# Performance work log

Hardware: AMD Instinct MI355X
Metric: run time of the kernel (lower is better)

## Reference

```python
import jax, jax.numpy as jnp
import numpy as np
import math

B, N, F = 16, 1024, 1024
OUT = 1024

def setup_inputs() -> dict:
    key = jax.random.key(0)
    k1, k2, k3, k4 = jax.random.split(key, 4)
    prott5_emd = jax.random.normal(k1, (B, N, F), dtype=jnp.float32)
    # shared (dense) normalized adjacency, as the original applies one adj to every sample
    adj = jax.random.uniform(k2, (N, N), dtype=jnp.float32)
    adj = adj / jnp.sum(adj, axis=1, keepdims=True)  # row-normalize like a GCN propagation matrix
    h0 = jax.random.normal(k3, (B, N, F), dtype=jnp.float32)
    stdv = 1.0 / math.sqrt(OUT)
    weight = jax.random.uniform(k4, (F, OUT), minval=-stdv, maxval=stdv, dtype=jnp.float32)
    return {"prott5_emd": prott5_emd, "adj": adj, "h0": h0, "weight": weight,
            "lamda": 0.5, "alpha": 0.1, "l": 1}

def reference(prott5_emd, adj, h0, weight, lamda, alpha, l):
    # GraphConvolution (GCNII-style), variant=False, residual=False
    theta = min(1.0, math.log(lamda / l + 1.0))  # static python scalar
    # batched aggregation: adj @ x_i for every sample i  ->  [B, N, F]
    hi = jnp.einsum('nm,bmf->bnf', adj, prott5_emd)
    support = (1.0 - alpha) * hi + alpha * h0          # affine combine with initial features
    out = theta * jnp.einsum('bnf,fo->bno', support, weight) + (1.0 - theta) * support
    return out
```

## Files before the change

### kernel.cpp

```cpp
#include <hip/hip_runtime.h>
#include <hip/hip_bf16.h>

typedef __attribute__((ext_vector_type(8))) short bf16x8;
typedef __attribute__((ext_vector_type(4))) float f32x4;
typedef __attribute__((ext_vector_type(4))) unsigned int u32x4;
typedef __attribute__((ext_vector_type(2))) unsigned int u32x2;

__device__ __forceinline__ float b2f(unsigned short u) {
  unsigned int x = ((unsigned int)u) << 16;
  float f;
  __builtin_memcpy(&f, &x, 4);
  return f;
}
__device__ __forceinline__ unsigned short f2b(float f) {
  __hip_bfloat16 h = __float2bfloat16(f);
  unsigned short u;
  __builtin_memcpy(&u, &h, 2);
  return u;
}

__global__ __launch_bounds__(256) void prep_all(
    const float* __restrict__ X, const float* __restrict__ adj,
    const float* __restrict__ W, unsigned short* __restrict__ XT,
    unsigned short* __restrict__ AJ, unsigned short* __restrict__ WT,
    float theta) {
  const int z = blockIdx.z;
  const int t = threadIdx.x;
  const int r0 = blockIdx.y * 64, c0 = blockIdx.x * 64;

  if (z == 17) {
#pragma unroll
    for (int p = 0; p < 4; ++p) {
      const int id = t + 256 * p;
      const int r = id >> 4, c4 = (id & 15) * 4;
      f32x4 v = *(const f32x4*)(adj + (size_t)(r0 + r) * 1024 + (c0 + c4));
      unsigned short o[4];
#pragma unroll
      for (int j = 0; j < 4; ++j) o[j] = f2b(v[j]);
      u32x2 pk;
      __builtin_memcpy(&pk, o, 8);
      *(u32x2*)(AJ + (size_t)(r0 + r) * 1024 + (c0 + c4)) = pk;
    }
    return;
  }

  if (z == 16) {
    __shared__ float tile[64][65];
#pragma unroll
    for (int p = 0; p < 4; ++p) {
      const int id = t + 256 * p;
      const int r = id >> 4, c4 = (id & 15) * 4;
      f32x4 v = *(const f32x4*)(W + (size_t)(r0 + r) * 1024 + (c0 + c4));
#pragma unroll
      for (int j = 0; j < 4; ++j) tile[r][c4 + j] = v[j];
    }
    __syncthreads();
#pragma unroll
    for (int p = 0; p < 2; ++p) {
      const int id = t + 256 * p;
      const int oc = id >> 3, cr8 = (id & 7) * 8;
      u32x4 v;
      unsigned short* pv = (unsigned short*)&v;
#pragma unroll
      for (int j = 0; j < 8; ++j) {
        const int o = c0 + oc, f = r0 + cr8 + j;
        float val = theta * tile[cr8 + j][oc] + (o == f ? (1.0f - theta) : 0.f);
        pv[j] = f2b(val);
      }
      *(u32x4*)(WT + (size_t)(c0 + oc) * 1024 + (r0 + cr8)) = v;
    }
    return;
  }

  __shared__ unsigned short tile[64][68];
  const float* s = X + (size_t)z * 1024 * 1024;
  unsigned short* d = XT + (size_t)z * 1024 * 1024;
#pragma unroll
  for (int p = 0; p < 4; ++p) {
    const int id = t + 256 * p;
    const int r = id >> 4, c4 = (id & 15) * 4;
    f32x4 v = *(const f32x4*)(s + (size_t)(r0 + r) * 1024 + (c0 + c4));
#pragma unroll
    for (int j = 0; j < 4; ++j) tile[r][c4 + j] = f2b(v[j]);
  }
  __syncthreads();
#pragma unroll
  for (int p = 0; p < 2; ++p) {
    const int id = t + 256 * p;
    const int oc = id >> 3, cr8 = (id & 7) * 8;
    u32x4 v;
    unsigned short* pv = (unsigned short*)&v;
#pragma unroll
    for (int j = 0; j < 8; ++j) pv[j] = tile[cr8 + j][oc];
    *(u32x4*)(d + (size_t)(c0 + oc) * 1024 + (r0 + cr8)) = v;
  }
}

__device__ __forceinline__ void stage_tile16(unsigned short* ldsbase,
                                             const unsigned short* __restrict__ gbase,
                                             size_t rowbase, int half, int k0,
                                             int t, int wv) {
#pragma unroll
  for (int l = 0; l < 2; ++l) {
    const int id = l * 512 + t;
    const int rl = id >> 3, c = id & 7;
    const int gc = (c ^ (rl & 7)) << 3;
    const unsigned short* g = gbase + (rowbase + half * 128 + rl) * 1024 + k0 + gc;
    unsigned short* dst = ldsbase + half * 8192 + (l * 512 + wv * 64) * 8;
    __builtin_amdgcn_global_load_lds(
        (const __attribute__((address_space(1))) unsigned int*)g,
        (__attribute__((address_space(3))) unsigned int*)dst, 16, 0, 0);
  }
}

#define LOAD_A(MH)                                                     \
  {                                                                    \
    const unsigned short* Ard = lds[rd * 2 + 0];                       \
    _Pragma("unroll") for (int mi = 0; mi < 4; ++mi)                   \
        _Pragma("unroll") for (int kk = 0; kk < 2; ++kk) {             \
      const int row = wm + (MH)*64 + mi * 16 + (lane & 15);            \
      const int ch = ((kk * 4 + (lane >> 4)) ^ (row & 7)) << 3;        \
      areg[mi][kk] = *(const bf16x8*)(Ard + row * 64 + ch);            \
    }                                                                  \
  }
#define LOAD_B(NH, BR)                                                 \
  {                                                                    \
    const unsigned short* Brd = lds[rd * 2 + 1];                       \
    _Pragma("unroll") for (int nj = 0; nj < 2; ++nj)                   \
        _Pragma("unroll") for (int kk = 0; kk < 2; ++kk) {             \
      const int row = wn + (NH)*32 + nj * 16 + (lane & 15);            \
      const int ch = ((kk * 4 + (lane >> 4)) ^ (row & 7)) << 3;        \
      BR[nj][kk] = *(const bf16x8*)(Brd + row * 64 + ch);              \
    }                                                                  \
  }
#define MFMA_Q(MH, NH, BR)                                             \
  do {                                                                 \
    __builtin_amdgcn_s_setprio(1);                                     \
    _Pragma("unroll") for (int mi = 0; mi < 4; ++mi)                   \
        _Pragma("unroll") for (int nj = 0; nj < 2; ++nj)               \
            _Pragma("unroll") for (int kk = 0; kk < 2; ++kk)           \
        acc[(MH)*4 + mi][(NH)*2 + nj] =                                \
        __builtin_amdgcn_mfma_f32_16x16x32_bf16(                       \
            areg[mi][kk], BR[nj][kk], acc[(MH)*4 + mi][(NH)*2 + nj],   \
            0, 0, 0);                                                  \
    __builtin_amdgcn_s_setprio(0);                                     \
  } while (0)
#define LGKM0                                          \
  asm volatile("s_waitcnt lgkmcnt(0)" ::: "memory");   \
  __builtin_amdgcn_sched_barrier(0)
#define BAR __builtin_amdgcn_s_barrier()

#define GEMM_KLOOP                                                            \
  for (int tt = 0; tt < NT; ++tt) {                                           \
    const int rd = tt & 1, wr = rd ^ 1;                                       \
    LOAD_A(0);                                                                \
    LOAD_B(0, b0r);                                                           \
    if (tt + 1 < NT)                                                          \
      stage_tile16(lds[wr * 2 + 1], BT, n0, 1, (tt + 1) * 64, t, wv);         \
    BAR; LGKM0; MFMA_Q(0, 0, b0r); BAR;                                       \
    LOAD_B(1, b1r);                                                           \
    if (tt + 1 < NT)                                                          \
      stage_tile16(lds[wr * 2 + 0], A, m0, 1, (tt + 1) * 64, t, wv);          \
    BAR; LGKM0; MFMA_Q(0, 1, b1r); BAR;                                       \
    LOAD_A(1);                                                                \
    if (tt + 2 < NT)                                                          \
      stage_tile16(lds[rd * 2 + 1], BT, n0, 0, (tt + 2) * 64, t, wv);         \
    BAR; LGKM0; MFMA_Q(1, 1, b1r); BAR;                                       \
    if (tt + 2 < NT)                                                          \
      stage_tile16(lds[rd * 2 + 0], A, m0, 0, (tt + 2) * 64, t, wv);          \
    BAR; LGKM0; MFMA_Q(1, 0, b0r);                                            \
    asm volatile("s_waitcnt vmcnt(4)" ::: "memory");                          \
    BAR;                                                                      \
  }

#define GEMM_PROLOGUE                                                         \
  stage_tile16(lds[0], A, m0, 0, 0, t, wv);                                   \
  stage_tile16(lds[0], A, m0, 1, 0, t, wv);                                   \
  stage_tile16(lds[1], BT, n0, 0, 0, t, wv);                                  \
  stage_tile16(lds[1], BT, n0, 1, 0, t, wv);                                  \
  stage_tile16(lds[3], BT, n0, 0, 64, t, wv);                                 \
  stage_tile16(lds[2], A, m0, 0, 64, t, wv);                                  \
  asm volatile("s_waitcnt vmcnt(4)" ::: "memory");                            \
  BAR;

#define EPI_DUMP_HALF(MH)                                                     \
  if ((wv >> 2) == (MH)) {                                                    \
    const int q = lane >> 4;                                                  \
    _Pragma("unroll") for (int mi = 0; mi < 8; ++mi)                          \
        _Pragma("unroll") for (int nj = 0; nj < 4; ++nj)                      \
            _Pragma("unroll") for (int r = 0; r < 4; ++r) {                   \
      const int row = mi * 16 + q * 4 + r;                                    \
      const int col = (wn + nj * 16 + (lane & 15)) ^ (q << 4);                \
      ldsF[row * 256 + col] = acc[mi][nj][r];                                 \
    }                                                                         \
  }

__global__ __launch_bounds__(512, 2) void gemm1(
    const unsigned short* __restrict__ A, const unsigned short* __restrict__ BT,
    const float* __restrict__ E, unsigned short* __restrict__ Cq,
    float c0, float c1) {
  constexpr int NT = 16;
  constexpr size_t NF = 1024ull * 1024ull;
  __shared__ unsigned short lds[4][16384];
  const int bid = blockIdx.x;
  const int nid = (bid & 7) * 32 + (bid >> 3);
  const size_t m0 = (size_t)(nid >> 6) * 256, n0 = (size_t)(nid & 63) * 256;
  const int t = threadIdx.x, lane = t & 63, wv = t >> 6;
  const int wm = (wv >> 2) * 128, wn = (wv & 3) * 64;

  f32x4 acc[8][4];
#pragma unroll
  for (int i = 0; i < 8; ++i)
#pragma unroll
    for (int j = 0; j < 4; ++j) acc[i][j] = (f32x4){0.f, 0.f, 0.f, 0.f};
  bf16x8 areg[4][2], b0r[2][2], b1r[2][2];

  GEMM_PROLOGUE
  GEMM_KLOOP

  const size_t base = (n0 >> 10) * NF + (n0 & 1023) + m0 * 1024;
  float* ldsF = (float*)lds;
#pragma unroll
  for (int MH = 0; MH < 2; ++MH) {
    __syncthreads();
    EPI_DUMP_HALF(MH)
    __syncthreads();
#pragma unroll 4
    for (int it = 0; it < 16; ++it) {
      const int chunk = it * 512 + t;
      const int row = chunk >> 6;
      const int c4 = (chunk & 63) * 4;
      const int sc4 = c4 ^ (((row >> 2) & 3) << 4);
      const f32x4 s = *(const f32x4*)(ldsF + row * 256 + sc4);
      const size_t goff = base + (size_t)(MH * 128 + row) * 1024 + c4;
      const f32x4 h = *(const f32x4*)(E + goff);
      unsigned short o[4];
#pragma unroll
      for (int j = 0; j < 4; ++j) o[j] = f2b(c0 * s[j] + c1 * h[j]);
      u32x2 pk;
      __builtin_memcpy(&pk, o, 8);
      *(u32x2*)(Cq + goff) = pk;
    }
  }
}

__global__ __launch_bounds__(512, 2) void gemm2(
    const unsigned short* __restrict__ A, const unsigned short* __restrict__ BT,
    float* __restrict__ Co) {
  constexpr int NT = 16;
  __shared__ unsigned short lds[4][16384];
  const int bid = blockIdx.x;
  const int nid = (bid & 7) * 32 + (bid >> 3);
  const size_t m0 = (size_t)(nid >> 2) * 256, n0 = (size_t)(nid & 3) * 256;
  const int t = threadIdx.x, lane = t & 63, wv = t >> 6;
  const int wm = (wv >> 2) * 128, wn = (wv & 3) * 64;

  f32x4 acc[8][4];
#pragma unroll
  for (int i = 0; i < 8; ++i)
#pragma unroll
    for (int j = 0; j < 4; ++j) acc[i][j] = (f32x4){0.f, 0.f, 0.f, 0.f};
  bf16x8 areg[4][2], b0r[2][2], b1r[2][2];

  GEMM_PROLOGUE
  GEMM_KLOOP

  const size_t base = m0 * 1024 + n0;
  float* ldsF = (float*)lds;
#pragma unroll
  for (int MH = 0; MH < 2; ++MH) {
    __syncthreads();
    EPI_DUMP_HALF(MH)
    __syncthreads();
#pragma unroll 4
    for (int it = 0; it < 16; ++it) {
      const int chunk = it * 512 + t;
      const int row = chunk >> 6;
      const int c4 = (chunk & 63) * 4;
      const int sc4 = c4 ^ (((row >> 2) & 3) << 4);
      const f32x4 s = *(const f32x4*)(ldsF + row * 256 + sc4);
      *(f32x4*)(Co + base + (size_t)(MH * 128 + row) * 1024 + c4) = s;
    }
  }
}

#undef LOAD_A
#undef LOAD_B
#undef MFMA_Q
#undef LGKM0
#undef BAR
#undef GEMM_KLOOP
#undef GEMM_PROLOGUE
#undef EPI_DUMP_HALF

extern "C" void kernel_launch(void* const* d_in, const int* in_sizes, int n_in,
                              void* d_out, int out_size, void* d_ws,
                              size_t ws_size, hipStream_t stream) {
  const float* X = (const float*)d_in[0];
  const float* adj = (const float*)d_in[1];
  const float* h0 = (const float*)d_in[2];
  const float* W = (const float*)d_in[3];
  float* out = (float*)d_out;

  const size_t NF = 1024ull * 1024ull;
  unsigned short* XT = (unsigned short*)d_ws;
  unsigned short* WT = XT + 16 * NF;
  unsigned short* AJ = WT + NF;
  unsigned short* S = AJ + NF;

  const float theta = 0.405465108f;

  prep_all<<<dim3(16, 16, 18), 256, 0, stream>>>(X, adj, W, XT, AJ, WT, theta);

  gemm1<<<dim3(256), 512, 0, stream>>>(AJ, XT, h0, S, 0.9f, 0.1f);
  gemm2<<<dim3(256), 512, 0, stream>>>(S, WT, out);
}
```

Measured before the change: 108.0 us.

## Replace gemm1 with smaller-tile single-buffered kernel using more blocks

The first GEMM (adj @ X plus h0 blend) is rewritten to use 128x128 output tiles with 256-thread blocks and 1024 blocks, single-buffered LDS staging with a full vmcnt(0) wait per k-step, and a simpler MFMA loop. The aim is more blocks and occupancy per CU, trading away the deep software pipelining of the 256x256 tile kernel. The risks are lower operand reuse per block, more global traffic, and exposed load latency from the synchronous staging. gemm2 is unchanged in behaviour; its macros are only inlined.

```diff
diff --git a/kernel.cpp b/kernel.cpp
--- a/kernel.cpp
+++ b/kernel.cpp
@@ -93,6 +93,119 @@
 #pragma unroll
     for (int j = 0; j < 8; ++j) pv[j] = tile[cr8 + j][oc];
     *(u32x4*)(d + (size_t)(c0 + oc) * 1024 + (r0 + cr8)) = v;
+  }
+}
+
+__global__ __launch_bounds__(256, 3) void gemm1(
+    const unsigned short* __restrict__ A, const unsigned short* __restrict__ BT,
+    const float* __restrict__ E, unsigned short* __restrict__ Cq,
+    float c0, float c1) {
+  constexpr int NT = 16;
+  constexpr size_t NF = 1024ull * 1024ull;
+  __shared__ unsigned short Abuf[128 * 64];
+  __shared__ unsigned short Bbuf[128 * 64];
+  const int bid = blockIdx.x;
+  const int nid = (bid & 7) * 128 + (bid >> 3);
+  const size_t m0 = (size_t)(nid >> 7) * 128, n0 = (size_t)(nid & 127) * 128;
+  const int t = threadIdx.x, lane = t & 63, wv = t >> 6;
+  const int wm = (wv >> 1) * 64, wn = (wv & 1) * 64;
+
+  f32x4 acc[4][4];
+#pragma unroll
+  for (int i = 0; i < 4; ++i)
+#pragma unroll
+    for (int j = 0; j < 4; ++j) acc[i][j] = (f32x4){0.f, 0.f, 0.f, 0.f};
+
+  for (int tt = 0; tt < NT; ++tt) {
+    const int k0 = tt * 64;
+#pragma unroll
+    for (int l = 0; l < 4; ++l) {
+      const int id = l * 256 + t;
+      const int rl = id >> 3, c = id & 7;
+      const int gc = (c ^ (rl & 7)) << 3;
+      const unsigned short* ga = A + (m0 + rl) * 1024 + k0 + gc;
+      __builtin_amdgcn_global_load_lds(
+          (const __attribute__((address_space(1))) unsigned int*)ga,
+          (__attribute__((address_space(3))) unsigned int*)(Abuf + id * 8),
+          16, 0, 0);
+    }
+#pragma unroll
+    for (int l = 0; l < 4; ++l) {
+      const int id = l * 256 + t;
+      const int rl = id >> 3, c = id & 7;
+      const int gc = (c ^ (rl & 7)) << 3;
+      const unsigned short* gb = BT + (n0 + rl) * 1024 + k0 + gc;
+      __builtin_amdgcn_global_load_lds(
+          (const __attribute__((address_space(1))) unsigned int*)gb,
+          (__attribute__((address_space(3))) unsigned int*)(Bbuf + id * 8),
+          16, 0, 0);
+    }
+    asm volatile("s_waitcnt vmcnt(0)" ::: "memory");
+    __builtin_amdgcn_s_barrier();
+
+    bf16x8 breg[4][2];
+#pragma unroll
+    for (int nj = 0; nj < 4; ++nj)
+#pragma unroll
+      for (int kk = 0; kk < 2; ++kk) {
+        const int row = wn + nj * 16 + (lane & 15);
+        const int ch = ((kk * 4 + (lane >> 4)) ^ (row & 7)) << 3;
+        breg[nj][kk] = *(const bf16x8*)(Bbuf + row * 64 + ch);
+      }
+#pragma unroll
+    for (int mi = 0; mi < 4; ++mi) {
+      bf16x8 ar[2];
+#pragma unroll
+      for (int kk = 0; kk < 2; ++kk) {
+        const int row = wm + mi * 16 + (lane & 15);
+        const int ch = ((kk * 4 + (lane >> 4)) ^ (row & 7)) << 3;
+        ar[kk] = *(const bf16x8*)(Abuf + row * 64 + ch);
+      }
+#pragma unroll
+      for (int nj = 0; nj < 4; ++nj)
+#pragma unroll
+        for (int kk = 0; kk < 2; ++kk)
+          acc[mi][nj] = __builtin_amdgcn_mfma_f32_16x16x32_bf16(
+              ar[kk], breg[nj][kk], acc[mi][nj], 0, 0, 0);
+    }
+    __builtin_amdgcn_s_barrier();
+  }
+
+  const size_t base = (n0 >> 10) * NF + (n0 & 1023) + m0 * 1024;
+  float* ldsF = (float*)Abuf;
+#pragma unroll
+  for (int NH = 0; NH < 2; ++NH) {
+    __syncthreads();
+    if ((wv & 1) == NH) {
+      const int q = lane >> 4;
+#pragma unroll
+      for (int mi = 0; mi < 4; ++mi)
+#pragma unroll
+        for (int nj = 0; nj < 4; ++nj)
+#pragma unroll
+          for (int r = 0; r < 4; ++r) {
+            const int row = wm + mi * 16 + q * 4 + r;
+            const int col = (nj * 16 + (lane & 15)) ^ (q << 4);
+            ldsF[row * 64 + col] = acc[mi][nj][r];
+          }
+    }
+    __syncthreads();
+#pragma unroll 4
+    for (int it = 0; it < 8; ++it) {
+      const int chunk = it * 256 + t;
+      const int row = chunk >> 4;
+      const int c4 = (chunk & 15) * 4;
+      const int sc4 = c4 ^ (((row >> 2) & 3) << 4);
+      const f32x4 s = *(const f32x4*)(ldsF + row * 64 + sc4);
+      const size_t goff = base + (size_t)row * 1024 + NH * 64 + c4;
+      const f32x4 h = *(const f32x4*)(E + goff);
+      unsigned short o[4];
+#pragma unroll
+      for (int j = 0; j < 4; ++j) o[j] = f2b(c0 * s[j] + c1 * h[j]);
+      u32x2 pk;
+      __builtin_memcpy(&pk, o, 8);
+      *(u32x2*)(Cq + goff) = pk;
+    }
   }
 }
 
@@ -150,100 +263,6 @@
   __builtin_amdgcn_sched_barrier(0)
 #define BAR __builtin_amdgcn_s_barrier()
 
-#define GEMM_KLOOP                                                            \
-  for (int tt = 0; tt < NT; ++tt) {                                           \
-    const int rd = tt & 1, wr = rd ^ 1;                                       \
-    LOAD_A(0);                                                                \
-    LOAD_B(0, b0r);                                                           \
-    if (tt + 1 < NT)                                                          \
-      stage_tile16(lds[wr * 2 + 1], BT, n0, 1, (tt + 1) * 64, t, wv);         \
-    BAR; LGKM0; MFMA_Q(0, 0, b0r); BAR;                                       \
-    LOAD_B(1, b1r);                                                           \
-    if (tt + 1 < NT)                                                          \
-      stage_tile16(lds[wr * 2 + 0], A, m0, 1, (tt + 1) * 64, t, wv);          \
-    BAR; LGKM0; MFMA_Q(0, 1, b1r); BAR;                                       \
-    LOAD_A(1);                                                                \
-    if (tt + 2 < NT)                                                          \
-      stage_tile16(lds[rd * 2 + 1], BT, n0, 0, (tt + 2) * 64, t, wv);         \
-    BAR; LGKM0; MFMA_Q(1, 1, b1r); BAR;                                       \
-    if (tt + 2 < NT)                                                          \
-      stage_tile16(lds[rd * 2 + 0], A, m0, 0, (tt + 2) * 64, t, wv);          \
-    BAR; LGKM0; MFMA_Q(1, 0, b0r);                                            \
-    asm volatile("s_waitcnt vmcnt(4)" ::: "memory");                          \
-    BAR;                                                                      \
-  }
-
-#define GEMM_PROLOGUE                                                         \
-  stage_tile16(lds[0], A, m0, 0, 0, t, wv);                                   \
-  stage_tile16(lds[0], A, m0, 1, 0, t, wv);                                   \
-  stage_tile16(lds[1], BT, n0, 0, 0, t, wv);                                  \
-  stage_tile16(lds[1], BT, n0, 1, 0, t, wv);                                  \
-  stage_tile16(lds[3], BT, n0, 0, 64, t, wv);                                 \
-  stage_tile16(lds[2], A, m0, 0, 64, t, wv);                                  \
-  asm volatile("s_waitcnt vmcnt(4)" ::: "memory");                            \
-  BAR;
-
-#define EPI_DUMP_HALF(MH)                                                     \
-  if ((wv >> 2) == (MH)) {                                                    \
-    const int q = lane >> 4;                                                  \
-    _Pragma("unroll") for (int mi = 0; mi < 8; ++mi)                          \
-        _Pragma("unroll") for (int nj = 0; nj < 4; ++nj)                      \
-            _Pragma("unroll") for (int r = 0; r < 4; ++r) {                   \
-      const int row = mi * 16 + q * 4 + r;                                    \
-      const int col = (wn + nj * 16 + (lane & 15)) ^ (q << 4);                \
-      ldsF[row * 256 + col] = acc[mi][nj][r];                                 \
-    }                                                                         \
-  }
-
-__global__ __launch_bounds__(512, 2) void gemm1(
-    const unsigned short* __restrict__ A, const unsigned short* __restrict__ BT,
-    const float* __restrict__ E, unsigned short* __restrict__ Cq,
-    float c0, float c1) {
-  constexpr int NT = 16;
-  constexpr size_t NF = 1024ull * 1024ull;
-  __shared__ unsigned short lds[4][16384];
-  const int bid = blockIdx.x;
-  const int nid = (bid & 7) * 32 + (bid >> 3);
-  const size_t m0 = (size_t)(nid >> 6) * 256, n0 = (size_t)(nid & 63) * 256;
-  const int t = threadIdx.x, lane = t & 63, wv = t >> 6;
-  const int wm = (wv >> 2) * 128, wn = (wv & 3) * 64;
-
-  f32x4 acc[8][4];
-#pragma unroll
-  for (int i = 0; i < 8; ++i)
-#pragma unroll
-    for (int j = 0; j < 4; ++j) acc[i][j] = (f32x4){0.f, 0.f, 0.f, 0.f};
-  bf16x8 areg[4][2], b0r[2][2], b1r[2][2];
-
-  GEMM_PROLOGUE
-  GEMM_KLOOP
-
-  const size_t base = (n0 >> 10) * NF + (n0 & 1023) + m0 * 1024;
-  float* ldsF = (float*)lds;
-#pragma unroll
-  for (int MH = 0; MH < 2; ++MH) {
-    __syncthreads();
-    EPI_DUMP_HALF(MH)
-    __syncthreads();
-#pragma unroll 4
-    for (int it = 0; it < 16; ++it) {
-      const int chunk = it * 512 + t;
-      const int row = chunk >> 6;
-      const int c4 = (chunk & 63) * 4;
-      const int sc4 = c4 ^ (((row >> 2) & 3) << 4);
-      const f32x4 s = *(const f32x4*)(ldsF + row * 256 + sc4);
-      const size_t goff = base + (size_t)(MH * 128 + row) * 1024 + c4;
-      const f32x4 h = *(const f32x4*)(E + goff);
-      unsigned short o[4];
-#pragma unroll
-      for (int j = 0; j < 4; ++j) o[j] = f2b(c0 * s[j] + c1 * h[j]);
-      u32x2 pk;
-      __builtin_memcpy(&pk, o, 8);
-      *(u32x2*)(Cq + goff) = pk;
-    }
-  }
-}
-
 __global__ __launch_bounds__(512, 2) void gemm2(
     const unsigned short* __restrict__ A, const unsigned short* __restrict__ BT,
     float* __restrict__ Co) {
@@ -262,15 +281,51 @@
     for (int j = 0; j < 4; ++j) acc[i][j] = (f32x4){0.f, 0.f, 0.f, 0.f};
   bf16x8 areg[4][2], b0r[2][2], b1r[2][2];
 
-  GEMM_PROLOGUE
-  GEMM_KLOOP
+  stage_tile16(lds[0], A, m0, 0, 0, t, wv);
+  stage_tile16(lds[0], A, m0, 1, 0, t, wv);
+  stage_tile16(lds[1], BT, n0, 0, 0, t, wv);
+  stage_tile16(lds[1], BT, n0, 1, 0, t, wv);
+  stage_tile16(lds[3], BT, n0, 0, 64, t, wv);
+  stage_tile16(lds[2], A, m0, 0, 64, t, wv);
+  asm volatile("s_waitcnt vmcnt(4)" ::: "memory");
+  BAR;
+
+  for (int tt = 0; tt < NT; ++tt) {
+    const int rd = tt & 1, wr = rd ^ 1;
+    LOAD_A(0);
+    LOAD_B(0, b0r);
+    if (tt + 1 < NT) stage_tile16(lds[wr * 2 + 1], BT, n0, 1, (tt + 1) * 64, t, wv);
+    BAR; LGKM0; MFMA_Q(0, 0, b0r); BAR;
+    LOAD_B(1, b1r);
+    if (tt + 1 < NT) stage_tile16(lds[wr * 2 + 0], A, m0, 1, (tt + 1) * 64, t, wv);
+    BAR; LGKM0; MFMA_Q(0, 1, b1r); BAR;
+    LOAD_A(1);
+    if (tt + 2 < NT) stage_tile16(lds[rd * 2 + 1], BT, n0, 0, (tt + 2) * 64, t, wv);
+    BAR; LGKM0; MFMA_Q(1, 1, b1r); BAR;
+    if (tt + 2 < NT) stage_tile16(lds[rd * 2 + 0], A, m0, 0, (tt + 2) * 64, t, wv);
+    BAR; LGKM0; MFMA_Q(1, 0, b0r);
+    asm volatile("s_waitcnt vmcnt(4)" ::: "memory");
+    BAR;
+  }
 
   const size_t base = m0 * 1024 + n0;
   float* ldsF = (float*)lds;
 #pragma unroll
   for (int MH = 0; MH < 2; ++MH) {
     __syncthreads();
-    EPI_DUMP_HALF(MH)
+    if ((wv >> 2) == MH) {
+      const int q = lane >> 4;
+#pragma unroll
+      for (int mi = 0; mi < 8; ++mi)
+#pragma unroll
+        for (int nj = 0; nj < 4; ++nj)
+#pragma unroll
+          for (int r = 0; r < 4; ++r) {
+            const int row = mi * 16 + q * 4 + r;
+            const int col = (wn + nj * 16 + (lane & 15)) ^ (q << 4);
+            ldsF[row * 256 + col] = acc[mi][nj][r];
+          }
+    }
     __syncthreads();
 #pragma unroll 4
     for (int it = 0; it < 16; ++it) {
@@ -289,9 +344,6 @@
 #undef MFMA_Q
 #undef LGKM0
 #undef BAR
-#undef GEMM_KLOOP
-#undef GEMM_PROLOGUE
-#undef EPI_DUMP_HALF
 
 extern "C" void kernel_launch(void* const* d_in, const int* in_sizes, int n_in,
                               void* d_out, int out_size, void* d_ws,
@@ -312,6 +364,6 @@
 
   prep_all<<<dim3(16, 16, 18), 256, 0, stream>>>(X, adj, W, XT, AJ, WT, theta);
 
-  gemm1<<<dim3(256), 512, 0, stream>>>(AJ, XT, h0, S, 0.9f, 0.1f);
+  gemm1<<<dim3(1024), 256, 0, stream>>>(AJ, XT, h0, S, 0.9f, 0.1f);
   gemm2<<<dim3(256), 512, 0, stream>>>(S, WT, out);
 }
```

Result: slower. 119.6 us (+10.7%).
